# Kernel tuning notes

Measured on AMD Instinct MI355X. Metric: run time of the kernel, lower is better.

The kernel has to match this reference:

```python
import jax, jax.numpy as jnp
import numpy as np
from jax import lax

B, N, D, E, P, K, H = 32, 512, 512, 8, 96, 25, 4
PAD = 12  # conv padding so length is preserved


def setup_inputs() -> dict:
    key = jax.random.key(0)
    ks = jax.random.split(key, 16)
    s = 0.05  # weight scale to keep softmax/cosine well-conditioned
    x = jax.random.normal(ks[0], (B, N, D), dtype=jnp.float32)
    router = jax.random.normal(ks[1], (1, E, D), dtype=jnp.float32)
    Wq = jax.random.normal(ks[2], (D, D), dtype=jnp.float32) * s
    bq = jax.random.normal(ks[3], (D,), dtype=jnp.float32) * s
    Wk = jax.random.normal(ks[4], (D, D), dtype=jnp.float32) * s
    bk = jax.random.normal(ks[5], (D,), dtype=jnp.float32) * s
    Wv = jax.random.normal(ks[6], (D, D), dtype=jnp.float32) * s
    bv = jax.random.normal(ks[7], (D,), dtype=jnp.float32) * s
    Wo = jax.random.normal(ks[8], (D, D), dtype=jnp.float32) * s
    bo = jax.random.normal(ks[9], (D,), dtype=jnp.float32) * s
    Wc = jax.random.normal(ks[10], (E, 2, K), dtype=jnp.float32) * s  # E experts' Conv1d(2,1,25) stacked as out-channels
    bc = jax.random.normal(ks[11], (E,), dtype=jnp.float32) * s
    Wp = jax.random.normal(ks[12], (E, D, P), dtype=jnp.float32) * s  # E experts' Linear(D,P), stored (in,out)
    bp = jax.random.normal(ks[13], (E, P), dtype=jnp.float32) * s
    return {"x": x, "router": router, "Wq": Wq, "bq": bq, "Wk": Wk, "bk": bk,
            "Wv": Wv, "bv": bv, "Wo": Wo, "bo": bo, "Wc": Wc, "bc": bc,
            "Wp": Wp, "bp": bp}


def _forward(x, router, Wq, bq, Wk, bk, Wv, bv, Wo, bo, Wc, bc, Wp, bp):
    b, n, d = x.shape
    e = router.shape[1]
    dk = d // H
    r = jnp.broadcast_to(router, (b, e, d))
    # multi-head attention: queries=router slots, keys/values=x (dropout = identity at eval)
    q = (r @ Wq + bq).reshape(b, e, H, dk)
    k = (x @ Wk + bk).reshape(b, n, H, dk)
    v = (x @ Wv + bv).reshape(b, n, H, dk)
    scale = 1.0 / jnp.sqrt(jnp.asarray(dk, x.dtype))
    scores = jnp.einsum('blhe,bshe->bhls', q, k)  # [b,H,e,n]
    A = jax.nn.softmax(scale * scores, axis=-1)
    att = jnp.einsum('bhls,bshd->blhd', A, v).reshape(b, e, d)
    att = att @ Wo + bo  # [b,e,d]
    # cosine-similarity routing score, mapped to (1+pi)/2
    dot = jnp.einsum('bed,bnd->ben', att, x)
    norm_a = jnp.linalg.norm(att, axis=2, keepdims=True)          # [b,e,1]
    norm_x = jnp.linalg.norm(x, axis=2)[:, None, :]                # [b,1,n]
    score = (1.0 + dot / (norm_a * norm_x)) / 2.0                  # [b,e,n]
    idx = jnp.argmax(score, axis=1)                                # [b,n] expert per token
    z = jnp.take_along_axis(att, idx[:, :, None], axis=1)          # [b,n,d]
    result = jnp.stack([x, z], axis=-2).reshape(b * n, 2, d)       # [bn,2,d]
    # run all E expert convs at once (experts stacked as output channels)
    conv_out = lax.conv_general_dilated(
        result, Wc, window_strides=(1,), padding=[(PAD, PAD)],
        dimension_numbers=('NCH', 'OIH', 'NCH')) + bc[None, :, None]  # [bn,E,d]
    lin = jnp.einsum('nel,elp->nep', conv_out, Wp) + bp[None]         # [bn,E,P]
    flat_idx = idx.reshape(-1)
    out = jnp.take_along_axis(lin, flat_idx[:, None, None], axis=1)[:, 0, :]
    return out.reshape(b, n, P)


def reference(x, router, Wq, bq, Wk, bk, Wv, bv, Wo, bo, Wc, bc, Wp, bp):
    return _forward(x, router, Wq, bq, Wk, bk, Wv, bv, Wo, bo, Wc, bc, Wp, bp)
```

## Files before the change

kernel.cpp:

```cpp
#include <hip/hip_runtime.h>
#include <hip/hip_bf16.h>

#define B_ 32
#define N_ 512
#define D_ 512
#define E_ 8
#define P_ 96
#define KC 25
#define H_ 4
#define DK 128
#define HE 32
#define BN 16384

typedef short short8 __attribute__((ext_vector_type(8)));
typedef float f32x4 __attribute__((ext_vector_type(4)));

#define OCNT  4096
#define OS2   4352
#define OM    5120
#define OC    21504
#define OA    21536
#define OATT  676896
#define OTOK  807968
#define OWEFF 939040
#define OZC   1332256
#define OA1   5551136
#define OAP   16777216

__device__ __forceinline__ float b2f(short s) {
  unsigned u = ((unsigned)(unsigned short)s) << 16;
  return __builtin_bit_cast(float, u);
}
__device__ __forceinline__ unsigned short f2b(float f) {
  return __builtin_bit_cast(unsigned short, __float2bfloat16(f));
}

__global__ __launch_bounds__(256) void k_head(const float* __restrict__ router,
        const float* __restrict__ Wq, const float* __restrict__ bq,
        const float* __restrict__ Wk, const float* __restrict__ bk,
        const float* __restrict__ Wp, const float* __restrict__ Wc,
        float* __restrict__ M, float* __restrict__ c,
        int* __restrict__ cnt, float* __restrict__ s2,
        __hip_bfloat16* __restrict__ weff) {
  __shared__ float sm[5824];
  int bid = blockIdx.x;
  int tid = threadIdx.x;
  if (bid < 64) {
    float* rs = sm;
    float* ps = sm + 512;
    float* qs = sm + 768;
    int he = bid >> 1, ch = bid & 1;
    int h = he >> 3, e = he & 7;
    for (int i = tid; i < 512; i += 256) rs[i] = router[e * D_ + i];
    __syncthreads();
    {
      int j = tid & 127, dh = tid >> 7;
      const float* wq = Wq + h * 128 + j;
      float acc = 0.f;
      for (int d = dh * 256; d < dh * 256 + 256; d += 4) {
        acc = fmaf(rs[d], wq[d * D_], acc);
        acc = fmaf(rs[d + 1], wq[(d + 1) * D_], acc);
        acc = fmaf(rs[d + 2], wq[(d + 2) * D_], acc);
        acc = fmaf(rs[d + 3], wq[(d + 3) * D_], acc);
      }
      ps[dh * 128 + j] = acc;
    }
    __syncthreads();
    if (tid < 128) qs[tid] = ps[tid] + ps[128 + tid] + bq[h * 128 + tid];
    __syncthreads();
    {
      int d0 = ch * 256 + tid;
      const float* wrow = Wk + d0 * D_ + h * 128;
      float acc = 0.f;
      for (int jj = 0; jj < 128; jj += 4) {
        float4 wv = *(const float4*)(wrow + jj);
        acc = fmaf(wv.x, qs[jj], acc);
        acc = fmaf(wv.y, qs[jj + 1], acc);
        acc = fmaf(wv.z, qs[jj + 2], acc);
        acc = fmaf(wv.w, qs[jj + 3], acc);
      }
      M[he * D_ + d0] = acc;
    }
    if (ch == 0 && tid < 64) {
      float s = qs[tid] * bk[h * 128 + tid] + qs[tid + 64] * bk[h * 128 + tid + 64];
#pragma unroll
      for (int off = 32; off; off >>= 1) s += __shfl_xor(s, off);
      if (tid == 0) c[he] = s;
    }
  } else if (bid < 192) {
    float* T = sm;
    float* wcs = sm + 5760;
    int eb = bid - 64;
    int e = eb >> 4, mc = eb & 15;
    int lo = mc * 32 - 12;
    for (int idx = tid; idx < 56 * 24; idx += 256) {
      int lp = idx / 24, p4 = (idx - lp * 24) * 4;
      int l = lo + lp;
      float4 v = {0.f, 0.f, 0.f, 0.f};
      if (l >= 0 && l < D_) v = *(const float4*)(Wp + (e * D_ + l) * P_ + p4);
      T[p4 * 60 + lp] = v.x; T[(p4 + 1) * 60 + lp] = v.y;
      T[(p4 + 2) * 60 + lp] = v.z; T[(p4 + 3) * 60 + lp] = v.w;
    }
    if (tid < 50) wcs[tid] = Wc[e * 2 * KC + tid];
    __syncthreads();
    int m = tid & 31, pg = tid >> 5;
#pragma unroll
    for (int j = 0; j < 2; ++j)
      for (int k2 = 0; k2 < 12; ++k2) {
        int p = pg * 12 + k2;
        float acc = 0.f;
#pragma unroll
        for (int k = 0; k < KC; ++k)
          acc = fmaf(wcs[j * 25 + k], T[p * 60 + m - k + 24], acc);
        weff[(((e * 2 + j) * P_ + p) << 9) + mc * 32 + m] = __float2bfloat16(acc);
      }
  } else {
    int e = bid - 192;
    if (bid == 192) cnt[tid] = 0;
    if (tid < 192) {
      int p = tid % 96, lg = tid / 96;
      float s = 0.f;
      const float* wp = Wp + e * D_ * P_ + p;
      for (int l = lg * 256; l < lg * 256 + 256; ++l) s += wp[l * P_];
      sm[lg * 96 + p] = s;
    }
    __syncthreads();
    if (tid < 96) s2[e * 96 + tid] = sm[tid] + sm[96 + tid];
  }
}

__global__ __launch_bounds__(128) void k_logits(const float* __restrict__ x,
        const float* __restrict__ M, float* __restrict__ A0,
        float* __restrict__ A1) {
  __shared__ float xs[64 * 132];
  __shared__ float Ms[32 * 132];
  int dh = blockIdx.x & 1;
  int nt8 = (blockIdx.x >> 1) & 7;
  int b = blockIdx.x >> 4;
  int tid = threadIdx.x;
  const float* xb = x + (b * N_ + nt8 * 64) * D_ + dh * 256;
  const float* Mb = M + dh * 256;
  float acc[4][4] = {{0.f}};
  for (int kc = 0; kc < 2; ++kc) {
    for (int idx = tid; idx < 2048; idx += 128) {
      int r = idx >> 5, c4 = (idx & 31) * 4;
      *(float4*)(xs + r * 132 + c4) = *(const float4*)(xb + r * D_ + kc * 128 + c4);
    }
    for (int idx = tid; idx < 1024; idx += 128) {
      int r = idx >> 5, c4 = (idx & 31) * 4;
      *(float4*)(Ms + r * 132 + c4) = *(const float4*)(Mb + r * D_ + kc * 128 + c4);
    }
    __syncthreads();
    int nt = tid & 15, ht = tid >> 4;
#pragma unroll 4
    for (int d4 = 0; d4 < 128; d4 += 4) {
      float4 xv[4], mv[4];
#pragma unroll
      for (int i = 0; i < 4; ++i)
        xv[i] = *(const float4*)(xs + (nt + 16 * i) * 132 + d4);
#pragma unroll
      for (int j = 0; j < 4; ++j)
        mv[j] = *(const float4*)(Ms + (ht + 8 * j) * 132 + d4);
#pragma unroll
      for (int i = 0; i < 4; ++i)
#pragma unroll
        for (int j = 0; j < 4; ++j) {
          float s = acc[i][j];
          s = fmaf(xv[i].x, mv[j].x, s);
          s = fmaf(xv[i].y, mv[j].y, s);
          s = fmaf(xv[i].z, mv[j].z, s);
          s = fmaf(xv[i].w, mv[j].w, s);
          acc[i][j] = s;
        }
    }
    __syncthreads();
  }
  int nt = tid & 15, ht = tid >> 4;
  float* Ad = dh ? A1 : A0;
#pragma unroll
  for (int j = 0; j < 4; ++j) {
    int he = ht + 8 * j;
#pragma unroll
    for (int i = 0; i < 4; ++i)
      Ad[(b * HE + he) * N_ + nt8 * 64 + nt + 16 * i] = acc[i][j];
  }
}

__global__ __launch_bounds__(512) void k_u(const float* __restrict__ x,
        const float* __restrict__ A0, const float* __restrict__ A1,
        const float* __restrict__ c, const float* __restrict__ Wv,
        const float* __restrict__ bv, float* __restrict__ ap) {
  __shared__ __align__(16) char smem[49248];
  float* Ast  = (float*)smem;
  float* part = (float*)(smem + 8192);
  float* ust  = (float*)(smem + 40960);
  float* mH   = (float*)(smem + 49152);
  float* sH   = (float*)(smem + 49184);
  float* mS   = (float*)(smem + 49216);
  float* iS   = (float*)(smem + 49232);
  int id = blockIdx.x;
  int b = id & 31, g = id >> 5;
  int h = g >> 1, eb = (g & 1) * 4;
  int tid = threadIdx.x;
  const float scale = 0.08838834764831845f;
  int wv = tid >> 6, lane = tid & 63;
  int he_l = wv >> 1, half = wv & 1;
  {
    int heg = g * 4 + he_l;
    const float* r0 = A0 + (b * HE + heg) * N_;
    const float* r1 = A1 + (b * HE + heg) * N_;
    float cc = c[heg];
    float v[4];
    float m = -1e30f;
#pragma unroll
    for (int k = 0; k < 4; ++k) {
      int n = half * 256 + lane + k * 64;
      float vv = scale * (r0[n] + r1[n] + cc);
      v[k] = vv;
      m = fmaxf(m, vv);
    }
    m = fmaxf(m, __shfl_xor(m, 1)); m = fmaxf(m, __shfl_xor(m, 2));
    m = fmaxf(m, __shfl_xor(m, 4)); m = fmaxf(m, __shfl_xor(m, 8));
    m = fmaxf(m, __shfl_xor(m, 16)); m = fmaxf(m, __shfl_xor(m, 32));
    if (lane == 0) mH[wv] = m;
    __syncthreads();
    m = fmaxf(mH[he_l * 2], mH[he_l * 2 + 1]);
    if (lane == 0 && half == 0) mS[he_l] = m;
    float s = 0.f;
#pragma unroll
    for (int k = 0; k < 4; ++k) s += expf(v[k] - m);
    s += __shfl_xor(s, 1); s += __shfl_xor(s, 2); s += __shfl_xor(s, 4);
    s += __shfl_xor(s, 8); s += __shfl_xor(s, 16); s += __shfl_xor(s, 32);
    if (lane == 0) sH[wv] = s;
    __syncthreads();
    if (lane == 0 && half == 0) iS[he_l] = 1.0f / (sH[he_l * 2] + sH[he_l * 2 + 1]);
  }
  __syncthreads();
  for (int idx = tid; idx < 2048; idx += 512) {
    int hl = idx >> 9, n = idx & 511;
    int heg = g * 4 + hl;
    float vv = scale * (A0[(b * HE + heg) * N_ + n] + A1[(b * HE + heg) * N_ + n]
                        + c[heg]);
    Ast[n * 4 + hl] = expf(vv - mS[hl]) * iS[hl];
  }
  __syncthreads();
  {
    int ns = tid >> 7, dg = tid & 127;
    float4 acc[4];
#pragma unroll
    for (int j = 0; j < 4; ++j) acc[j] = (float4){0.f, 0.f, 0.f, 0.f};
    const float* xb = x + (b * N_ + ns * 128) * D_ + dg * 4;
    const float* ab = Ast + ns * 128 * 4;
#pragma unroll 4
    for (int n = 0; n < 128; ++n) {
      float4 xv = *(const float4*)(xb + n * D_);
      float4 av = *(const float4*)(ab + n * 4);
      acc[0].x = fmaf(av.x, xv.x, acc[0].x); acc[0].y = fmaf(av.x, xv.y, acc[0].y);
      acc[0].z = fmaf(av.x, xv.z, acc[0].z); acc[0].w = fmaf(av.x, xv.w, acc[0].w);
      acc[1].x = fmaf(av.y, xv.x, acc[1].x); acc[1].y = fmaf(av.y, xv.y, acc[1].y);
      acc[1].z = fmaf(av.y, xv.z, acc[1].z); acc[1].w = fmaf(av.y, xv.w, acc[1].w);
      acc[2].x = fmaf(av.z, xv.x, acc[2].x); acc[2].y = fmaf(av.z, xv.y, acc[2].y);
      acc[2].z = fmaf(av.z, xv.z, acc[2].z); acc[2].w = fmaf(av.z, xv.w, acc[2].w);
      acc[3].x = fmaf(av.w, xv.x, acc[3].x); acc[3].y = fmaf(av.w, xv.y, acc[3].y);
      acc[3].z = fmaf(av.w, xv.z, acc[3].z); acc[3].w = fmaf(av.w, xv.w, acc[3].w);
    }
#pragma unroll
    for (int j = 0; j < 4; ++j)
      *(float4*)(part + ns * 2048 + j * 512 + dg * 4) = acc[j];
  }
  __syncthreads();
  {
    int d = tid;
    float4 s = {0.f, 0.f, 0.f, 0.f};
#pragma unroll
    for (int ns2 = 0; ns2 < 4; ++ns2) {
      s.x += part[ns2 * 2048 + 0 * 512 + d];
      s.y += part[ns2 * 2048 + 1 * 512 + d];
      s.z += part[ns2 * 2048 + 2 * 512 + d];
      s.w += part[ns2 * 2048 + 3 * 512 + d];
    }
    *(float4*)(ust + d * 4) = s;
  }
  __syncthreads();
  {
    int kq = tid >> 5, cg = tid & 31, c4 = cg * 4;
    float4 a2[4];
#pragma unroll
    for (int j = 0; j < 4; ++j) a2[j] = (float4){0.f, 0.f, 0.f, 0.f};
    const float* wvp = Wv + h * 128 + c4;
#pragma unroll 4
    for (int d = kq * 32; d < kq * 32 + 32; ++d) {
      float4 w4 = *(const float4*)(wvp + d * D_);
      float4 uu = *(const float4*)(ust + d * 4);
      a2[0].x = fmaf(uu.x, w4.x, a2[0].x); a2[0].y = fmaf(uu.x, w4.y, a2[0].y);
      a2[0].z = fmaf(uu.x, w4.z, a2[0].z); a2[0].w = fmaf(uu.x, w4.w, a2[0].w);
      a2[1].x = fmaf(uu.y, w4.x, a2[1].x); a2[1].y = fmaf(uu.y, w4.y, a2[1].y);
      a2[1].z = fmaf(uu.y, w4.z, a2[1].z); a2[1].w = fmaf(uu.y, w4.w, a2[1].w);
      a2[2].x = fmaf(uu.z, w4.x, a2[2].x); a2[2].y = fmaf(uu.z, w4.y, a2[2].y);
      a2[2].z = fmaf(uu.z, w4.z, a2[2].z); a2[2].w = fmaf(uu.z, w4.w, a2[2].w);
      a2[3].x = fmaf(uu.w, w4.x, a2[3].x); a2[3].y = fmaf(uu.w, w4.y, a2[3].y);
      a2[3].z = fmaf(uu.w, w4.z, a2[3].z); a2[3].w = fmaf(uu.w, w4.w, a2[3].w);
    }
#pragma unroll
    for (int j = 0; j < 4; ++j)
      *(float4*)(part + kq * 512 + j * 128 + c4) = a2[j];
  }
  __syncthreads();
  {
    int j = tid >> 7, cc = tid & 127;
    float s = 0.f;
#pragma unroll
    for (int kq2 = 0; kq2 < 16; ++kq2) s += part[kq2 * 512 + j * 128 + cc];
    ap[(b * E_ + eb + j) * D_ + h * 128 + cc] = s + bv[h * 128 + cc];
  }
}

__global__ __launch_bounds__(512) void k_op(const float* __restrict__ ap,
        const float* __restrict__ Wo, const float* __restrict__ bo,
        float* __restrict__ att) {
  __shared__ __align__(16) char smem[40960];
  float* apt  = (float*)smem;
  float* part = (float*)(smem + 8192);
  int id = blockIdx.x;
  int b = id & 31, q2 = id >> 5;
  int cq = q2 >> 1, eh = q2 & 1;
  int tid = threadIdx.x;
  {
    int j = tid >> 7, tl = tid & 127;
    const float* arow = ap + (b * E_ + eh * 4 + j) * D_;
#pragma unroll
    for (int k = 0; k < 4; ++k) {
      int i = tl + k * 128;
      apt[i * 4 + j] = arow[i];
    }
  }
  __syncthreads();
  {
    int kq = tid >> 5, cg = tid & 31, c4 = cg * 4;
    float4 a2[4];
#pragma unroll
    for (int j = 0; j < 4; ++j) a2[j] = (float4){0.f, 0.f, 0.f, 0.f};
    const float* wop = Wo + cq * 128 + c4;
#pragma unroll 4
    for (int d = kq * 32; d < kq * 32 + 32; ++d) {
      float4 w4 = *(const float4*)(wop + d * D_);
      float4 uu = *(const float4*)(apt + d * 4);
      a2[0].x = fmaf(uu.x, w4.x, a2[0].x); a2[0].y = fmaf(uu.x, w4.y, a2[0].y);
      a2[0].z = fmaf(uu.x, w4.z, a2[0].z); a2[0].w = fmaf(uu.x, w4.w, a2[0].w);
      a2[1].x = fmaf(uu.y, w4.x, a2[1].x); a2[1].y = fmaf(uu.y, w4.y, a2[1].y);
      a2[1].z = fmaf(uu.y, w4.z, a2[1].z); a2[1].w = fmaf(uu.y, w4.w, a2[1].w);
      a2[2].x = fmaf(uu.z, w4.x, a2[2].x); a2[2].y = fmaf(uu.z, w4.y, a2[2].y);
      a2[2].z = fmaf(uu.z, w4.z, a2[2].z); a2[2].w = fmaf(uu.z, w4.w, a2[2].w);
      a2[3].x = fmaf(uu.w, w4.x, a2[3].x); a2[3].y = fmaf(uu.w, w4.y, a2[3].y);
      a2[3].z = fmaf(uu.w, w4.z, a2[3].z); a2[3].w = fmaf(uu.w, w4.w, a2[3].w);
    }
#pragma unroll
    for (int j = 0; j < 4; ++j)
      *(float4*)(part + kq * 512 + j * 128 + c4) = a2[j];
  }
  __syncthreads();
  {
    int j = tid >> 7, cc = tid & 127;
    float s = 0.f;
#pragma unroll
    for (int kq2 = 0; kq2 < 16; ++kq2) s += part[kq2 * 512 + j * 128 + cc];
    att[(b * E_ + eh * 4 + j) * D_ + cq * 128 + cc] = s + bo[cq * 128 + cc];
  }
}

__global__ __launch_bounds__(256) void k_route2(const float* __restrict__ x,
        const float* __restrict__ att, const __hip_bfloat16* __restrict__ weff,
        const float* __restrict__ s2, const float* __restrict__ bc,
        const float* __restrict__ bp, int* __restrict__ cnt,
        int* __restrict__ tok, float* __restrict__ zc) {
  __shared__ float att_s[8 * D_];
  __shared__ float rn[8];
  __shared__ float red[4][520];
  __shared__ int blist[8][32];
  __shared__ int bcnt[8];
  int b = blockIdx.x >> 4, tile = blockIdx.x & 15;
  for (int idx = threadIdx.x; idx < 1024; idx += 256)
    *(float4*)(att_s + idx * 4) = *(const float4*)(att + b * E_ * D_ + idx * 4);
  if (threadIdx.x < 8) bcnt[threadIdx.x] = 0;
  __syncthreads();
  {
    int e = threadIdx.x >> 5, l = threadIdx.x & 31;
    float s = 0.f;
    for (int d0 = l; d0 < D_; d0 += 32) {
      float v = att_s[e * D_ + d0];
      s = fmaf(v, v, s);
    }
#pragma unroll
    for (int off = 16; off; off >>= 1) s += __shfl_xor(s, off);
    if (l == 0) rn[e] = 1.0f / sqrtf(s);
  }
  __syncthreads();
  int w = threadIdx.x >> 6, lane = threadIdx.x & 63;
  int e2 = lane & 7, ch = lane >> 3;
  float* rw = red[w];
  for (int i = 0; i < 8; ++i) {
    int t = b * N_ + tile * 32 + w * 8 + i;
    const float* xp = x + t * D_ + lane * 8;
    float4 xa = *(const float4*)xp;
    float4 xb4 = *(const float4*)(xp + 4);
    float p[8];
#pragma unroll
    for (int e = 0; e < 8; ++e) {
      const float* apt = att_s + e * D_ + lane * 8;
      float4 a0 = *(const float4*)apt;
      float4 a1 = *(const float4*)(apt + 4);
      float s = a0.x * xa.x;
      s = fmaf(a0.y, xa.y, s); s = fmaf(a0.z, xa.z, s); s = fmaf(a0.w, xa.w, s);
      s = fmaf(a1.x, xb4.x, s); s = fmaf(a1.y, xb4.y, s);
      s = fmaf(a1.z, xb4.z, s); s = fmaf(a1.w, xb4.w, s);
      p[e] = s;
    }
#pragma unroll
    for (int e = 0; e < 8; ++e) rw[e * 65 + lane] = p[e];
    float s = 0.f;
#pragma unroll
    for (int k = 0; k < 8; ++k) s += rw[e2 * 65 + ch * 8 + k];
    s += __shfl_xor(s, 8); s += __shfl_xor(s, 16); s += __shfl_xor(s, 32);
    float sc = s * rn[e2];
    int be = e2;
#pragma unroll
    for (int off = 1; off < 8; off <<= 1) {
      float o = __shfl_xor(sc, off);
      int oe = __shfl_xor(be, off);
      if (o > sc || (o == sc && oe < be)) { sc = o; be = oe; }
    }
    if (lane == 0) {
      int slot = atomicAdd(&bcnt[be], 1);
      blist[be][slot] = t;
    }
  }
  __syncthreads();
  {
    int e = threadIdx.x >> 5, r = threadIdx.x & 31;
    int ce = bcnt[e];
    int gs = 0;
    if (r == 0 && ce > 0) gs = atomicAdd(&cnt[e * 32], ce);
    gs = __shfl(gs, (threadIdx.x & 63) & 32);
    for (int k2 = r; k2 < ce; k2 += 32) tok[e * BN + gs + k2] = blist[e][k2];
  }
  int grp = threadIdx.x >> 4, l16 = threadIdx.x & 15;
  for (int r = 0; r < 3; ++r) {
    int P = tile * 48 + r * 16 + grp;
    int ez = P / 96, p = P - ez * 96;
    const short* wrow = (const short*)weff + (((ez * 2 + 1) * P_ + p) << 9);
    const float* arow = att_s + ez * D_;
    float acc = 0.f;
#pragma unroll
    for (int seg = 0; seg < 4; ++seg) {
      int d = seg * 128 + l16 * 8;
      short8 w8 = *(const short8*)(wrow + d);
      const float* a8 = arow + d;
      acc = fmaf(a8[0], b2f(w8[0]), acc); acc = fmaf(a8[1], b2f(w8[1]), acc);
      acc = fmaf(a8[2], b2f(w8[2]), acc); acc = fmaf(a8[3], b2f(w8[3]), acc);
      acc = fmaf(a8[4], b2f(w8[4]), acc); acc = fmaf(a8[5], b2f(w8[5]), acc);
      acc = fmaf(a8[6], b2f(w8[6]), acc); acc = fmaf(a8[7], b2f(w8[7]), acc);
    }
    acc += __shfl_xor(acc, 1); acc += __shfl_xor(acc, 2);
    acc += __shfl_xor(acc, 4); acc += __shfl_xor(acc, 8);
    if (l16 == 0)
      zc[(b * E_ + ez) * P_ + p] = acc + bc[ez] * s2[ez * 96 + p] + bp[ez * 96 + p];
  }
}

__global__ __launch_bounds__(256) void k_final(const float* __restrict__ x,
        const __hip_bfloat16* __restrict__ weff, const float* __restrict__ zc,
        const int* __restrict__ cnt, const int* __restrict__ tok,
        float* __restrict__ out) {
  __shared__ __align__(16) unsigned short xsb[32 * 520];
  __shared__ int toks[32];
  int g = blockIdx.x;
  int cl_e[E_], bs[E_ + 1];
  bs[0] = 0;
#pragma unroll
  for (int e = 0; e < E_; ++e) {
    cl_e[e] = cnt[e * 32];
    bs[e + 1] = bs[e] + ((cl_e[e] + 31) >> 5);
  }
  if (g >= bs[E_]) return;
  int e = 0;
#pragma unroll
  for (int k = 1; k < E_; ++k) if (g >= bs[k]) e = k;
  int base = (g - bs[e]) * 32;
  int cnt_e = cl_e[e];
  int cl = cnt_e - base; if (cl > 32) cl = 32;
  int tid = threadIdx.x;
  if (tid < 32) toks[tid] = (tid < cl) ? tok[e * BN + base + tid] : tok[e * BN + base];
  __syncthreads();
  for (int idx = tid; idx < 32 * 128; idx += 256) {
    int r = idx >> 7, c4 = (idx & 127) * 4;
    float4 v = *(const float4*)(x + toks[r] * D_ + c4);
    ushort4 u4;
    u4.x = f2b(v.x); u4.y = f2b(v.y); u4.z = f2b(v.z); u4.w = f2b(v.w);
    *(ushort4*)(xsb + r * 520 + c4) = u4;
  }
  __syncthreads();
  int wave = tid >> 6, lane = tid & 63;
  int mw = wave & 1, nw = wave >> 1;
  int m16 = lane & 15, quad = lane >> 4;
  const short* w0 = (const short*)(weff + (e * 2 + 0) * P_ * D_);
  f32x4 acc[3];
#pragma unroll
  for (int nt = 0; nt < 3; ++nt) acc[nt] = (f32x4){0.f, 0.f, 0.f, 0.f};
  const short* arow = (const short*)xsb + (mw * 16 + m16) * 520 + quad * 8;
  const short* brow = w0 + (nw * 48 + m16) * D_ + quad * 8;
  for (int kt = 0; kt < 16; ++kt) {
    int koff = kt * 32;
    short8 a = *(const short8*)(arow + koff);
#pragma unroll
    for (int nt = 0; nt < 3; ++nt) {
      short8 bf = *(const short8*)(brow + nt * 16 * D_ + koff);
      acc[nt] = __builtin_amdgcn_mfma_f32_16x16x32_bf16(a, bf, acc[nt], 0, 0, 0);
    }
  }
#pragma unroll
  for (int nt = 0; nt < 3; ++nt)
#pragma unroll
    for (int rr = 0; rr < 4; ++rr) {
      int row = mw * 16 + quad * 4 + rr;
      if (row < cl) {
        int tg = toks[row];
        int bb = tg >> 9;
        int p = nw * 48 + nt * 16 + m16;
        out[tg * P_ + p] = acc[nt][rr] + zc[(bb * E_ + e) * P_ + p];
      }
    }
}

extern "C" void kernel_launch(void* const* d_in, const int* in_sizes, int n_in,
                              void* d_out, int out_size, void* d_ws, size_t ws_size,
                              hipStream_t stream) {
  const float* x      = (const float*)d_in[0];
  const float* router = (const float*)d_in[1];
  const float* Wq     = (const float*)d_in[2];
  const float* bq     = (const float*)d_in[3];
  const float* Wk     = (const float*)d_in[4];
  const float* bk     = (const float*)d_in[5];
  const float* Wv     = (const float*)d_in[6];
  const float* bv     = (const float*)d_in[7];
  const float* Wo     = (const float*)d_in[8];
  const float* bo     = (const float*)d_in[9];
  const float* Wc     = (const float*)d_in[10];
  const float* bc     = (const float*)d_in[11];
  const float* Wp     = (const float*)d_in[12];
  const float* bp     = (const float*)d_in[13];
  float* out = (float*)d_out;
  float* w = (float*)d_ws;

  int*   cnt  = (int*)(w + OCNT);
  float* s2   = w + OS2;
  float* M    = w + OM;
  float* c    = w + OC;
  float* A0   = w + OA;
  float* A1   = w + OA1;
  float* att  = w + OATT;
  int*   tok  = (int*)(w + OTOK);
  __hip_bfloat16* weff = (__hip_bfloat16*)(w + OWEFF);
  float* zc   = w + OZC;
  float* ap   = w + OAP;

  k_head<<<200, 256, 0, stream>>>(router, Wq, bq, Wk, bk, Wp, Wc, M, c, cnt, s2, weff);
  k_logits<<<512, 128, 0, stream>>>(x, M, A0, A1);
  k_u<<<256, 512, 0, stream>>>(x, A0, A1, c, Wv, bv, ap);
  k_op<<<256, 512, 0, stream>>>(ap, Wo, bo, att);
  k_route2<<<512, 256, 0, stream>>>(x, att, weff, s2, bc, bp, cnt, tok, zc);
  k_final<<<520, 256, 0, stream>>>(x, weff, zc, cnt, tok, out);
}
```

Measured before the change: 208.7 us.

## Move weff conv-folding into k_u blocks, fuse softmax reuse, enlarge route2 blocks

Result: faster. 199.1 us (-4.6%).

```diff
diff --git a/kernel.cpp b/kernel.cpp
--- a/kernel.cpp
+++ b/kernel.cpp
@@ -38,11 +38,10 @@
 __global__ __launch_bounds__(256) void k_head(const float* __restrict__ router,
         const float* __restrict__ Wq, const float* __restrict__ bq,
         const float* __restrict__ Wk, const float* __restrict__ bk,
-        const float* __restrict__ Wp, const float* __restrict__ Wc,
+        const float* __restrict__ Wp,
         float* __restrict__ M, float* __restrict__ c,
-        int* __restrict__ cnt, float* __restrict__ s2,
-        __hip_bfloat16* __restrict__ weff) {
-  __shared__ float sm[5824];
+        int* __restrict__ cnt, float* __restrict__ s2) {
+  __shared__ float sm[896];
   int bid = blockIdx.x;
   int tid = threadIdx.x;
   if (bid < 64) {
@@ -87,36 +86,9 @@
       for (int off = 32; off; off >>= 1) s += __shfl_xor(s, off);
       if (tid == 0) c[he] = s;
     }
-  } else if (bid < 192) {
-    float* T = sm;
-    float* wcs = sm + 5760;
-    int eb = bid - 64;
-    int e = eb >> 4, mc = eb & 15;
-    int lo = mc * 32 - 12;
-    for (int idx = tid; idx < 56 * 24; idx += 256) {
-      int lp = idx / 24, p4 = (idx - lp * 24) * 4;
-      int l = lo + lp;
-      float4 v = {0.f, 0.f, 0.f, 0.f};
-      if (l >= 0 && l < D_) v = *(const float4*)(Wp + (e * D_ + l) * P_ + p4);
-      T[p4 * 60 + lp] = v.x; T[(p4 + 1) * 60 + lp] = v.y;
-      T[(p4 + 2) * 60 + lp] = v.z; T[(p4 + 3) * 60 + lp] = v.w;
-    }
-    if (tid < 50) wcs[tid] = Wc[e * 2 * KC + tid];
-    __syncthreads();
-    int m = tid & 31, pg = tid >> 5;
-#pragma unroll
-    for (int j = 0; j < 2; ++j)
-      for (int k2 = 0; k2 < 12; ++k2) {
-        int p = pg * 12 + k2;
-        float acc = 0.f;
-#pragma unroll
-        for (int k = 0; k < KC; ++k)
-          acc = fmaf(wcs[j * 25 + k], T[p * 60 + m - k + 24], acc);
-        weff[(((e * 2 + j) * P_ + p) << 9) + mc * 32 + m] = __float2bfloat16(acc);
-      }
   } else {
-    int e = bid - 192;
-    if (bid == 192) cnt[tid] = 0;
+    int e = bid - 64;
+    if (bid == 64) cnt[tid] = 0;
     if (tid < 192) {
       int p = tid % 96, lg = tid / 96;
       float s = 0.f;
@@ -189,22 +161,54 @@
 __global__ __launch_bounds__(512) void k_u(const float* __restrict__ x,
         const float* __restrict__ A0, const float* __restrict__ A1,
         const float* __restrict__ c, const float* __restrict__ Wv,
-        const float* __restrict__ bv, float* __restrict__ ap) {
+        const float* __restrict__ bv, const float* __restrict__ Wp,
+        const float* __restrict__ Wc, __hip_bfloat16* __restrict__ weff,
+        float* __restrict__ ap) {
   __shared__ __align__(16) char smem[49248];
+  int tid = threadIdx.x;
+  if (blockIdx.x >= 256) {
+    float* T = (float*)smem;
+    float* wcs = (float*)smem + 5760;
+    int eb = blockIdx.x - 256;
+    int e = eb >> 4, mc = eb & 15;
+    int lo = mc * 32 - 12;
+    for (int idx = tid; idx < 56 * 24; idx += 512) {
+      int lp = idx / 24, p4 = (idx - lp * 24) * 4;
+      int l = lo + lp;
+      float4 v = {0.f, 0.f, 0.f, 0.f};
+      if (l >= 0 && l < D_) v = *(const float4*)(Wp + (e * D_ + l) * P_ + p4);
+      T[p4 * 60 + lp] = v.x; T[(p4 + 1) * 60 + lp] = v.y;
+      T[(p4 + 2) * 60 + lp] = v.z; T[(p4 + 3) * 60 + lp] = v.w;
+    }
+    if (tid < 50) wcs[tid] = Wc[e * 2 * KC + tid];
+    __syncthreads();
+    if (tid < 256) {
+      int m = tid & 31, pg = tid >> 5;
+#pragma unroll
+      for (int j = 0; j < 2; ++j)
+        for (int k2 = 0; k2 < 12; ++k2) {
+          int p = pg * 12 + k2;
+          float acc = 0.f;
+#pragma unroll
+          for (int k = 0; k < KC; ++k)
+            acc = fmaf(wcs[j * 25 + k], T[p * 60 + m - k + 24], acc);
+          weff[(((e * 2 + j) * P_ + p) << 9) + mc * 32 + m] = __float2bfloat16(acc);
+        }
+    }
+    return;
+  }
   float* Ast  = (float*)smem;
   float* part = (float*)(smem + 8192);
   float* ust  = (float*)(smem + 40960);
   float* mH   = (float*)(smem + 49152);
   float* sH   = (float*)(smem + 49184);
-  float* mS   = (float*)(smem + 49216);
-  float* iS   = (float*)(smem + 49232);
   int id = blockIdx.x;
   int b = id & 31, g = id >> 5;
-  int h = g >> 1, eb = (g & 1) * 4;
-  int tid = threadIdx.x;
+  int h = g >> 1, eb2 = (g & 1) * 4;
   const float scale = 0.08838834764831845f;
   int wv = tid >> 6, lane = tid & 63;
   int he_l = wv >> 1, half = wv & 1;
+  float p[4];
   {
     int heg = g * 4 + he_l;
     const float* r0 = A0 + (b * HE + heg) * N_;
@@ -225,23 +229,21 @@
     if (lane == 0) mH[wv] = m;
     __syncthreads();
     m = fmaxf(mH[he_l * 2], mH[he_l * 2 + 1]);
-    if (lane == 0 && half == 0) mS[he_l] = m;
     float s = 0.f;
 #pragma unroll
-    for (int k = 0; k < 4; ++k) s += expf(v[k] - m);
+    for (int k = 0; k < 4; ++k) { p[k] = expf(v[k] - m); s += p[k]; }
     s += __shfl_xor(s, 1); s += __shfl_xor(s, 2); s += __shfl_xor(s, 4);
     s += __shfl_xor(s, 8); s += __shfl_xor(s, 16); s += __shfl_xor(s, 32);
     if (lane == 0) sH[wv] = s;
-    __syncthreads();
-    if (lane == 0 && half == 0) iS[he_l] = 1.0f / (sH[he_l * 2] + sH[he_l * 2 + 1]);
-  }
-  __syncthreads();
-  for (int idx = tid; idx < 2048; idx += 512) {
-    int hl = idx >> 9, n = idx & 511;
-    int heg = g * 4 + hl;
-    float vv = scale * (A0[(b * HE + heg) * N_ + n] + A1[(b * HE + heg) * N_ + n]
-                        + c[heg]);
-    Ast[n * 4 + hl] = expf(vv - mS[hl]) * iS[hl];
+  }
+  __syncthreads();
+  {
+    float is_ = 1.0f / (sH[he_l * 2] + sH[he_l * 2 + 1]);
+#pragma unroll
+    for (int k = 0; k < 4; ++k) {
+      int n = half * 256 + lane + k * 64;
+      Ast[n * 4 + he_l] = p[k] * is_;
+    }
   }
   __syncthreads();
   {
@@ -311,7 +313,7 @@
     float s = 0.f;
 #pragma unroll
     for (int kq2 = 0; kq2 < 16; ++kq2) s += part[kq2 * 512 + j * 128 + cc];
-    ap[(b * E_ + eb + j) * D_ + h * 128 + cc] = s + bv[h * 128 + cc];
+    ap[(b * E_ + eb2 + j) * D_ + h * 128 + cc] = s + bv[h * 128 + cc];
   }
 }
 
@@ -368,23 +370,24 @@
   }
 }
 
-__global__ __launch_bounds__(256) void k_route2(const float* __restrict__ x,
+__global__ __launch_bounds__(512) void k_route2(const float* __restrict__ x,
         const float* __restrict__ att, const __hip_bfloat16* __restrict__ weff,
         const float* __restrict__ s2, const float* __restrict__ bc,
         const float* __restrict__ bp, int* __restrict__ cnt,
         int* __restrict__ tok, float* __restrict__ zc) {
   __shared__ float att_s[8 * D_];
   __shared__ float rn[8];
-  __shared__ float red[4][520];
-  __shared__ int blist[8][32];
+  __shared__ float red[8][520];
+  __shared__ int blist[8][64];
   __shared__ int bcnt[8];
-  int b = blockIdx.x >> 4, tile = blockIdx.x & 15;
-  for (int idx = threadIdx.x; idx < 1024; idx += 256)
+  int b = blockIdx.x >> 3, tile = blockIdx.x & 7;
+  int tid = threadIdx.x;
+  for (int idx = tid; idx < 1024; idx += 512)
     *(float4*)(att_s + idx * 4) = *(const float4*)(att + b * E_ * D_ + idx * 4);
-  if (threadIdx.x < 8) bcnt[threadIdx.x] = 0;
-  __syncthreads();
-  {
-    int e = threadIdx.x >> 5, l = threadIdx.x & 31;
+  if (tid < 8) bcnt[tid] = 0;
+  __syncthreads();
+  if (tid < 256) {
+    int e = tid >> 5, l = tid & 31;
     float s = 0.f;
     for (int d0 = l; d0 < D_; d0 += 32) {
       float v = att_s[e * D_ + d0];
@@ -395,11 +398,11 @@
     if (l == 0) rn[e] = 1.0f / sqrtf(s);
   }
   __syncthreads();
-  int w = threadIdx.x >> 6, lane = threadIdx.x & 63;
+  int w = tid >> 6, lane = tid & 63;
   int e2 = lane & 7, ch = lane >> 3;
   float* rw = red[w];
   for (int i = 0; i < 8; ++i) {
-    int t = b * N_ + tile * 32 + w * 8 + i;
+    int t = b * N_ + tile * 64 + w * 8 + i;
     const float* xp = x + t * D_ + lane * 8;
     float4 xa = *(const float4*)xp;
     float4 xb4 = *(const float4*)(xp + 4);
@@ -435,20 +438,19 @@
     }
   }
   __syncthreads();
-  {
-    int e = threadIdx.x >> 5, r = threadIdx.x & 31;
+  if (tid < 256) {
+    int e = tid >> 5, r = tid & 31;
     int ce = bcnt[e];
     int gs = 0;
     if (r == 0 && ce > 0) gs = atomicAdd(&cnt[e * 32], ce);
-    gs = __shfl(gs, (threadIdx.x & 63) & 32);
+    gs = __shfl(gs, (tid & 63) & 32);
     for (int k2 = r; k2 < ce; k2 += 32) tok[e * BN + gs + k2] = blist[e][k2];
   }
-  int grp = threadIdx.x >> 4, l16 = threadIdx.x & 15;
+  int grp = tid >> 4, l16 = tid & 15;
+  const float* arow = att_s + tile * D_;
   for (int r = 0; r < 3; ++r) {
-    int P = tile * 48 + r * 16 + grp;
-    int ez = P / 96, p = P - ez * 96;
-    const short* wrow = (const short*)weff + (((ez * 2 + 1) * P_ + p) << 9);
-    const float* arow = att_s + ez * D_;
+    int p = r * 32 + grp;
+    const short* wrow = (const short*)weff + (((tile * 2 + 1) * P_ + p) << 9);
     float acc = 0.f;
 #pragma unroll
     for (int seg = 0; seg < 4; ++seg) {
@@ -463,7 +465,8 @@
     acc += __shfl_xor(acc, 1); acc += __shfl_xor(acc, 2);
     acc += __shfl_xor(acc, 4); acc += __shfl_xor(acc, 8);
     if (l16 == 0)
-      zc[(b * E_ + ez) * P_ + p] = acc + bc[ez] * s2[ez * 96 + p] + bp[ez * 96 + p];
+      zc[(b * E_ + tile) * P_ + p] = acc + bc[tile] * s2[tile * 96 + p]
+                                     + bp[tile * 96 + p];
   }
 }
 
@@ -563,10 +566,10 @@
   float* zc   = w + OZC;
   float* ap   = w + OAP;
 
-  k_head<<<200, 256, 0, stream>>>(router, Wq, bq, Wk, bk, Wp, Wc, M, c, cnt, s2, weff);
+  k_head<<<72, 256, 0, stream>>>(router, Wq, bq, Wk, bk, Wp, M, c, cnt, s2);
   k_logits<<<512, 128, 0, stream>>>(x, M, A0, A1);
-  k_u<<<256, 512, 0, stream>>>(x, A0, A1, c, Wv, bv, ap);
+  k_u<<<384, 512, 0, stream>>>(x, A0, A1, c, Wv, bv, Wp, Wc, weff, ap);
   k_op<<<256, 512, 0, stream>>>(ap, Wo, bo, att);
-  k_route2<<<512, 256, 0, stream>>>(x, att, weff, s2, bc, bp, cnt, tok, zc);
+  k_route2<<<256, 512, 0, stream>>>(x, att, weff, s2, bc, bp, cnt, tok, zc);
   k_final<<<520, 256, 0, stream>>>(x, weff, zc, cnt, tok, out);
 }
```
